# Kernel optimization log

Hardware: AMD Instinct MI355X
Metric: run time of the kernel (lower is better)

Reference implementation:

```python
import jax, jax.numpy as jnp
import numpy as np

H, W = 256, 256
L = 1024
R = 4
B = 64
EPS = 1e-4
FF = (H + W) * R * 4


def setup_inputs() -> dict:
    key = jax.random.key(0)
    ks = jax.random.split(key, 8)
    x = jax.random.normal(ks[0], (B, L), dtype=jnp.float32)
    # Linear weights (torch Linear: out = x @ W.T), kaiming-uniform-ish init
    lim = 1.0 / np.sqrt(L)
    W_t = jax.random.uniform(ks[1], (FF, L), minval=-lim, maxval=lim, dtype=jnp.float32)
    W_g = jax.random.uniform(ks[2], (FF, L), minval=-lim, maxval=lim, dtype=jnp.float32)
    # weights_static: [2, H, W, 2]
    k_lim = np.sqrt(6.0 / (H * W))
    ws0 = jax.random.uniform(ks[3], (1, H, W, 2), minval=-k_lim, maxval=k_lim, dtype=jnp.float32)
    ws1_re = jax.random.uniform(ks[4], (1, H, W, 1), minval=EPS - 1.0, maxval=1.0 - EPS, dtype=jnp.float32)
    ws1_im = jax.random.uniform(ks[5], (1, H, W, 1), minval=-EPS, maxval=EPS, dtype=jnp.float32)
    weights_static = jnp.concatenate([ws0, jnp.concatenate([ws1_re, ws1_im], axis=-1)], axis=0)
    x_lim = np.sqrt(6.0 / (H + W))
    weights_mod = jax.random.uniform(ks[6], (4, H, W), minval=-x_lim, maxval=x_lim, dtype=jnp.float32)
    c_lim = 1.0 / np.sqrt(R)
    kc1, kc2 = jax.random.split(ks[7])
    conv_w = jax.random.uniform(kc1, (R, R), minval=-c_lim, maxval=c_lim, dtype=jnp.float32)  # [out_ch, in_ch] for 1x1 conv
    conv_b = jax.random.uniform(kc2, (R,), minval=-c_lim, maxval=c_lim, dtype=jnp.float32)
    return {"x": x, "W_t": W_t, "W_g": W_g, "weights_static": weights_static,
            "weights_mod": weights_mod, "conv_w": conv_w, "conv_b": conv_b}


def reference(x, W_t, W_g, weights_static, weights_mod, conv_w, conv_b):
    b = x.shape[0]
    xt = x @ W_t.T                                  # [B, FF]
    xg = x @ W_g.T
    xg = xg * jax.nn.sigmoid(xg)                    # SiLU-style gate
    mod = xt * xg
    mod = mod.reshape(b, 4, -1)
    mod = mod / jnp.sqrt(jnp.mean(jnp.abs(mod), axis=-1, keepdims=True) + EPS)
    mod = mod.reshape(b, 4, R, H + W)
    a_part = mod[..., :H]                           # [B,4,R,H]
    b_part = mod[..., H:]                           # [B,4,R,W]
    outer = jnp.einsum('bkri,bkrj->bkrij', a_part, b_part)  # [B,4,R,H,W]
    # 1x1 conv (R->R) followed by sum over output channels collapses to a
    # single contraction with column-summed weights + summed bias (same math).
    w_eff = conv_w.sum(axis=0)                      # [R]
    b_eff = conv_b.sum()
    mod = jnp.einsum('bkrij,r->bkij', outer, w_eff) + b_eff  # [B,4,H,W]
    mod = weights_mod[None] * mod
    A0 = weights_static[0]                          # [H,W,2]
    A1 = weights_static[1]                          # [H,W,2]
    Bc = jnp.moveaxis(mod[:, 0:2], 1, -1)           # [B,H,W,2]
    re = A1[..., 0] * Bc[..., 0] - A1[..., 1] * Bc[..., 1]
    im = A1[..., 0] * Bc[..., 1] - A1[..., 1] * Bc[..., 0]
    mag = jnp.sqrt(re * re + im * im + EPS)         # [B,H,W]
    mag = jnp.sqrt(jnp.mean(mag, axis=(-1, -2)) + EPS)  # [B]
    inv = 1.0 / mag[:, None, None]
    mw_re = A0[..., 0] + re * inv                   # [B,H,W]
    mw_im = A0[..., 1] + im * inv
    proj = jnp.moveaxis(mod[:, 2:4], 1, -1)         # [B,H,W,2]
    den = jnp.sqrt(proj[..., 0] ** 2 + proj[..., 1] ** 2 + EPS)
    theta_cos = proj[..., 0] / den
    theta_sin = proj[..., 1] / den
    return mw_re * theta_cos + mw_im * theta_sin    # [B,H,W]
```

## Files before the change

kernel.cpp:

```cpp
#include <hip/hip_runtime.h>

typedef __bf16 bf16x8 __attribute__((ext_vector_type(8)));
typedef float floatx4 __attribute__((ext_vector_type(4)));

__device__ inline void cvt8_hl(const float* __restrict__ p, bf16x8& h, bf16x8& l){
  float4 v0 = *reinterpret_cast<const float4*>(p);
  float4 v1 = *reinterpret_cast<const float4*>(p + 4);
  float v[8] = {v0.x, v0.y, v0.z, v0.w, v1.x, v1.y, v1.z, v1.w};
  #pragma unroll
  for (int i = 0; i < 8; ++i) {
    __bf16 hi = (__bf16)v[i];
    h[i] = hi;
    l[i] = (__bf16)(v[i] - (float)hi);
  }
}

__global__ __launch_bounds__(256) void k1_gemm(
    const float* __restrict__ x,
    const float* __restrict__ Wt,
    const float* __restrict__ Wg,
    float* __restrict__ mod)
{
  __shared__ float red[3][32][64];
  const int tid  = threadIdx.x;
  const int wave = tid >> 6, lane = tid & 63;
  const int quad = lane >> 4, r16 = lane & 15;
  const int ff = blockIdx.x * 16 + r16;
  const int kb = wave * 256 + quad * 8;

  floatx4 accT[4], accG[4];
  #pragma unroll
  for (int m = 0; m < 4; ++m) { accT[m] = (floatx4)0.0f; accG[m] = (floatx4)0.0f; }

  const float* wt = Wt + ff * 1024 + kb;
  const float* wg = Wg + ff * 1024 + kb;
  const float* xp = x  + r16 * 1024 + kb;

  #pragma unroll
  for (int it = 0; it < 8; ++it) {
    const int ko = it * 32;
    bf16x8 bth, btl, bgh, bgl;
    cvt8_hl(wt + ko, bth, btl);
    cvt8_hl(wg + ko, bgh, bgl);
    #pragma unroll
    for (int mt = 0; mt < 4; ++mt) {
      bf16x8 ah, al;
      cvt8_hl(xp + mt * 16384 + ko, ah, al);
      accT[mt] = __builtin_amdgcn_mfma_f32_16x16x32_bf16(ah, bth, accT[mt], 0, 0, 0);
      accT[mt] = __builtin_amdgcn_mfma_f32_16x16x32_bf16(ah, btl, accT[mt], 0, 0, 0);
      accT[mt] = __builtin_amdgcn_mfma_f32_16x16x32_bf16(al, bth, accT[mt], 0, 0, 0);
      accG[mt] = __builtin_amdgcn_mfma_f32_16x16x32_bf16(ah, bgh, accG[mt], 0, 0, 0);
      accG[mt] = __builtin_amdgcn_mfma_f32_16x16x32_bf16(ah, bgl, accG[mt], 0, 0, 0);
      accG[mt] = __builtin_amdgcn_mfma_f32_16x16x32_bf16(al, bgh, accG[mt], 0, 0, 0);
    }
  }

  if (wave != 0) {
    #pragma unroll
    for (int mt = 0; mt < 4; ++mt)
      #pragma unroll
      for (int r = 0; r < 4; ++r) {
        red[wave - 1][mt * 4 + r][lane]      = accT[mt][r];
        red[wave - 1][16 + mt * 4 + r][lane] = accG[mt][r];
      }
  }
  __syncthreads();
  if (wave == 0) {
    #pragma unroll
    for (int mt = 0; mt < 4; ++mt) {
      #pragma unroll
      for (int r = 0; r < 4; ++r) {
        float t = accT[mt][r] + red[0][mt * 4 + r][lane]
                              + red[1][mt * 4 + r][lane]
                              + red[2][mt * 4 + r][lane];
        float g = accG[mt][r] + red[0][16 + mt * 4 + r][lane]
                              + red[1][16 + mt * 4 + r][lane]
                              + red[2][16 + mt * 4 + r][lane];
        float sig = 1.0f / (1.0f + __expf(-g));
        int b = mt * 16 + quad * 4 + r;
        mod[b * 8192 + ff] = t * g * sig;
      }
    }
  }
}

__global__ __launch_bounds__(256) void k1b_scale(const float* __restrict__ mod,
                                                 float* __restrict__ s)
{
  const int row = blockIdx.x;
  const int tid = threadIdx.x;
  const float* p = mod + row * 2048;
  float sum = 0.0f;
  #pragma unroll
  for (int q = 0; q < 8; ++q) sum += fabsf(p[q * 256 + tid]);
  #pragma unroll
  for (int o = 1; o < 64; o <<= 1) sum += __shfl_xor(sum, o, 64);
  __shared__ float ls[4];
  if ((tid & 63) == 0) ls[tid >> 6] = sum;
  __syncthreads();
  if (tid == 0) {
    float t = ls[0] + ls[1] + ls[2] + ls[3];
    s[row] = rsqrtf(t * (1.0f / 2048.0f) + 1e-4f);
  }
}

__global__ __launch_bounds__(256) void k2_mag(
    const float* __restrict__ mod, const float* __restrict__ s,
    const float* __restrict__ wstat,
    const float* __restrict__ wmod,
    const float* __restrict__ cw,
    const float* __restrict__ cb,
    float* __restrict__ partial)
{
  const int b = blockIdx.x, jc = blockIdx.y;
  const int tid = threadIdx.x;
  __shared__ __align__(16) float a_l[256 * 8];

  float weff[4]; float beff = 0.0f;
  #pragma unroll
  for (int r = 0; r < 4; ++r) {
    weff[r] = cw[r] + cw[4 + r] + cw[8 + r] + cw[12 + r];
    beff += cb[r];
  }
  const float s0 = s[b * 4 + 0], s1 = s[b * 4 + 1];
  const float* mb = mod + b * 8192;

  #pragma unroll
  for (int p = 0; p < 8; ++p) {
    int k = p >> 2, r = p & 3;
    float sc = (k ? s1 : s0) * weff[r];
    a_l[tid * 8 + p] = mb[k * 2048 + r * 512 + tid] * sc;
  }
  const int j = jc * 32 + (tid & 31);
  float bp[8];
  #pragma unroll
  for (int p = 0; p < 8; ++p) {
    int k = p >> 2, r = p & 3;
    bp[p] = mb[k * 2048 + r * 512 + 256 + j] * (k ? s1 : s0);
  }
  __syncthreads();

  const int ioff = tid >> 5;
  float acc = 0.0f;
  for (int it = 0; it < 32; ++it) {
    const int i = it * 8 + ioff;
    const float4 av0 = *reinterpret_cast<const float4*>(&a_l[i * 8]);
    const float4 av1 = *reinterpret_cast<const float4*>(&a_l[i * 8 + 4]);
    float d0 = av0.x * bp[0] + av0.y * bp[1] + av0.z * bp[2] + av0.w * bp[3];
    float d1 = av1.x * bp[4] + av1.y * bp[5] + av1.z * bp[6] + av1.w * bp[7];
    const int ij = i * 256 + j;
    float m0 = wmod[ij] * (d0 + beff);
    float m1 = wmod[65536 + ij] * (d1 + beff);
    float2 a1 = *reinterpret_cast<const float2*>(wstat + 131072 + ij * 2);
    float re = a1.x * m0 - a1.y * m1;
    float im = a1.x * m1 - a1.y * m0;
    acc += sqrtf(re * re + im * im + 1e-4f);
  }
  #pragma unroll
  for (int o = 1; o < 64; o <<= 1) acc += __shfl_xor(acc, o, 64);
  __shared__ float wsum[4];
  if ((tid & 63) == 0) wsum[tid >> 6] = acc;
  __syncthreads();
  if (tid == 0) partial[b * 8 + jc] = wsum[0] + wsum[1] + wsum[2] + wsum[3];
}

__global__ __launch_bounds__(256) void k4_out(
    const float* __restrict__ mod, const float* __restrict__ s,
    const float* __restrict__ wstat,
    const float* __restrict__ wmod,
    const float* __restrict__ cw,
    const float* __restrict__ cb,
    const float* __restrict__ partial,
    float* __restrict__ out)
{
  const int b = blockIdx.x, ibase = blockIdx.y * 32;
  const int tid = threadIdx.x;
  __shared__ __align__(16) float a_l[32 * 16];

  float weff[4]; float beff = 0.0f;
  #pragma unroll
  for (int r = 0; r < 4; ++r) {
    weff[r] = cw[r] + cw[4 + r] + cw[8 + r] + cw[12 + r];
    beff += cb[r];
  }
  float sk[4];
  #pragma unroll
  for (int k = 0; k < 4; ++k) sk[k] = s[b * 4 + k];
  const float* mb = mod + b * 8192;

  float tot = 0.0f;
  #pragma unroll
  for (int t = 0; t < 8; ++t) tot += partial[b * 8 + t];
  const float inv = rsqrtf(tot * (1.0f / 65536.0f) + 1e-4f);

  #pragma unroll
  for (int p = 0; p < 2; ++p) {
    int idx = p * 256 + tid;
    int il = idx & 31, kr = idx >> 5;
    int k = kr >> 2, r = kr & 3;
    a_l[il * 16 + kr] = mb[k * 2048 + r * 512 + ibase + il] * (sk[k] * weff[r]);
  }
  const int j = (tid & 127) * 2;
  const int ioff = tid >> 7;
  float bp0[16], bp1[16];
  #pragma unroll
  for (int kr = 0; kr < 16; ++kr) {
    int k = kr >> 2, r = kr & 3;
    float2 v = *reinterpret_cast<const float2*>(mb + k * 2048 + r * 512 + 256 + j);
    bp0[kr] = v.x * sk[k]; bp1[kr] = v.y * sk[k];
  }
  __syncthreads();

  #pragma unroll 2
  for (int it = 0; it < 16; ++it) {
    const int il = it * 2 + ioff;
    const int i = ibase + il;
    const float4 a0 = *reinterpret_cast<const float4*>(&a_l[il * 16]);
    const float4 a1 = *reinterpret_cast<const float4*>(&a_l[il * 16 + 4]);
    const float4 a2 = *reinterpret_cast<const float4*>(&a_l[il * 16 + 8]);
    const float4 a3 = *reinterpret_cast<const float4*>(&a_l[il * 16 + 12]);
    const int ij = i * 256 + j;
    const float2 wm0 = *reinterpret_cast<const float2*>(wmod + ij);
    const float2 wm1 = *reinterpret_cast<const float2*>(wmod + 65536 + ij);
    const float2 wm2 = *reinterpret_cast<const float2*>(wmod + 131072 + ij);
    const float2 wm3 = *reinterpret_cast<const float2*>(wmod + 196608 + ij);
    const float4 A0v = *reinterpret_cast<const float4*>(wstat + ij * 2);
    const float4 A1v = *reinterpret_cast<const float4*>(wstat + 131072 + ij * 2);
    float outv[2];
    #pragma unroll
    for (int e = 0; e < 2; ++e) {
      const float* bp = e ? bp1 : bp0;
      float d0 = a0.x * bp[0] + a0.y * bp[1] + a0.z * bp[2] + a0.w * bp[3];
      float d1 = a1.x * bp[4] + a1.y * bp[5] + a1.z * bp[6] + a1.w * bp[7];
      float d2 = a2.x * bp[8] + a2.y * bp[9] + a2.z * bp[10] + a2.w * bp[11];
      float d3 = a3.x * bp[12] + a3.y * bp[13] + a3.z * bp[14] + a3.w * bp[15];
      float m0 = (e ? wm0.y : wm0.x) * (d0 + beff);
      float m1 = (e ? wm1.y : wm1.x) * (d1 + beff);
      float m2 = (e ? wm2.y : wm2.x) * (d2 + beff);
      float m3 = (e ? wm3.y : wm3.x) * (d3 + beff);
      float A0r = e ? A0v.z : A0v.x;
      float A0i = e ? A0v.w : A0v.y;
      float A1r = e ? A1v.z : A1v.x;
      float A1i = e ? A1v.w : A1v.y;
      float re = A1r * m0 - A1i * m1;
      float im = A1r * m1 - A1i * m0;
      float mwre = A0r + re * inv;
      float mwim = A0i + im * inv;
      float rd = rsqrtf(m2 * m2 + m3 * m3 + 1e-4f);
      outv[e] = (mwre * m2 + mwim * m3) * rd;
    }
    *reinterpret_cast<float2*>(out + b * 65536 + ij) = make_float2(outv[0], outv[1]);
  }
}

extern "C" void kernel_launch(void* const* d_in, const int* in_sizes, int n_in,
                              void* d_out, int out_size, void* d_ws, size_t ws_size,
                              hipStream_t stream) {
  const float* x     = (const float*)d_in[0];
  const float* Wt    = (const float*)d_in[1];
  const float* Wg    = (const float*)d_in[2];
  const float* wstat = (const float*)d_in[3];
  const float* wmod  = (const float*)d_in[4];
  const float* cw    = (const float*)d_in[5];
  const float* cb    = (const float*)d_in[6];

  float* mod     = (float*)d_ws;
  float* sbuf    = mod + 524288;
  float* partial = sbuf + 256;

  k1_gemm  <<<512, 256, 0, stream>>>(x, Wt, Wg, mod);
  k1b_scale<<<256, 256, 0, stream>>>(mod, sbuf);
  k2_mag   <<<dim3(64, 8), 256, 0, stream>>>(mod, sbuf, wstat, wmod, cw, cb, partial);
  k4_out   <<<dim3(64, 8), 256, 0, stream>>>(mod, sbuf, wstat, wmod, cw, cb, partial,
                                             (float*)d_out);
}
```

Baseline: 152.1 us.

## Stage GEMM weights through LDS with async loads and fuse abs-sum reduction

Restructures the projection GEMM to use 512-thread blocks, where waves split the batch into 4 tiles and K into 2 halves. Weight tiles are loaded into swizzled, double-buffered LDS via global_load_lds, so they are fetched once per block instead of once per wave. The per-row |mod| sums are now accumulated with atomics in the GEMM epilogue, which removes the separate scale kernel. The consumers compute rsqrt themselves, and a memset is added to clear the sums. This cuts one launch and the redundant weight traffic, at the cost of atomics, an extra memset, and order-dependent float summation.

```diff
diff --git a/kernel.cpp b/kernel.cpp
--- a/kernel.cpp
+++ b/kernel.cpp
@@ -3,9 +3,7 @@
 typedef __bf16 bf16x8 __attribute__((ext_vector_type(8)));
 typedef float floatx4 __attribute__((ext_vector_type(4)));
 
-__device__ inline void cvt8_hl(const float* __restrict__ p, bf16x8& h, bf16x8& l){
-  float4 v0 = *reinterpret_cast<const float4*>(p);
-  float4 v1 = *reinterpret_cast<const float4*>(p + 4);
+__device__ inline void cvt8v(float4 v0, float4 v1, bf16x8& h, bf16x8& l){
   float v[8] = {v0.x, v0.y, v0.z, v0.w, v1.x, v1.y, v1.z, v1.w};
   #pragma unroll
   for (int i = 0; i < 8; ++i) {
@@ -15,97 +13,118 @@
   }
 }
 
-__global__ __launch_bounds__(256) void k1_gemm(
+__device__ inline void gload_lds16(const float* g, float* l){
+  __builtin_amdgcn_global_load_lds(
+      (const __attribute__((address_space(1))) unsigned int*)g,
+      (__attribute__((address_space(3))) unsigned int*)l, 16, 0, 0);
+}
+
+__global__ __launch_bounds__(512, 4) void k1_gemm(
     const float* __restrict__ x,
     const float* __restrict__ Wt,
     const float* __restrict__ Wg,
-    float* __restrict__ mod)
+    float* __restrict__ mod,
+    float* __restrict__ sums)
 {
-  __shared__ float red[3][32][64];
-  const int tid  = threadIdx.x;
-  const int wave = tid >> 6, lane = tid & 63;
-  const int quad = lane >> 4, r16 = lane & 15;
-  const int ff = blockIdx.x * 16 + r16;
-  const int kb = wave * 256 + quad * 8;
-
-  floatx4 accT[4], accG[4];
-  #pragma unroll
-  for (int m = 0; m < 4; ++m) { accT[m] = (floatx4)0.0f; accG[m] = (floatx4)0.0f; }
-
-  const float* wt = Wt + ff * 1024 + kb;
-  const float* wg = Wg + ff * 1024 + kb;
-  const float* xp = x  + r16 * 1024 + kb;
-
-  #pragma unroll
-  for (int it = 0; it < 8; ++it) {
-    const int ko = it * 32;
-    bf16x8 bth, btl, bgh, bgl;
-    cvt8_hl(wt + ko, bth, btl);
-    cvt8_hl(wg + ko, bgh, bgl);
-    #pragma unroll
-    for (int mt = 0; mt < 4; ++mt) {
-      bf16x8 ah, al;
-      cvt8_hl(xp + mt * 16384 + ko, ah, al);
-      accT[mt] = __builtin_amdgcn_mfma_f32_16x16x32_bf16(ah, bth, accT[mt], 0, 0, 0);
-      accT[mt] = __builtin_amdgcn_mfma_f32_16x16x32_bf16(ah, btl, accT[mt], 0, 0, 0);
-      accT[mt] = __builtin_amdgcn_mfma_f32_16x16x32_bf16(al, bth, accT[mt], 0, 0, 0);
-      accG[mt] = __builtin_amdgcn_mfma_f32_16x16x32_bf16(ah, bgh, accG[mt], 0, 0, 0);
-      accG[mt] = __builtin_amdgcn_mfma_f32_16x16x32_bf16(ah, bgl, accG[mt], 0, 0, 0);
-      accG[mt] = __builtin_amdgcn_mfma_f32_16x16x32_bf16(al, bgh, accG[mt], 0, 0, 0);
-    }
-  }
-
-  if (wave != 0) {
-    #pragma unroll
-    for (int mt = 0; mt < 4; ++mt)
-      #pragma unroll
-      for (int r = 0; r < 4; ++r) {
-        red[wave - 1][mt * 4 + r][lane]      = accT[mt][r];
-        red[wave - 1][16 + mt * 4 + r][lane] = accG[mt][r];
-      }
-  }
-  __syncthreads();
-  if (wave == 0) {
-    #pragma unroll
-    for (int mt = 0; mt < 4; ++mt) {
-      #pragma unroll
-      for (int r = 0; r < 4; ++r) {
-        float t = accT[mt][r] + red[0][mt * 4 + r][lane]
-                              + red[1][mt * 4 + r][lane]
-                              + red[2][mt * 4 + r][lane];
-        float g = accG[mt][r] + red[0][16 + mt * 4 + r][lane]
-                              + red[1][16 + mt * 4 + r][lane]
-                              + red[2][16 + mt * 4 + r][lane];
-        float sig = 1.0f / (1.0f + __expf(-g));
-        int b = mt * 16 + quad * 4 + r;
-        mod[b * 8192 + ff] = t * g * sig;
-      }
-    }
-  }
-}
-
-__global__ __launch_bounds__(256) void k1b_scale(const float* __restrict__ mod,
-                                                 float* __restrict__ s)
-{
-  const int row = blockIdx.x;
-  const int tid = threadIdx.x;
-  const float* p = mod + row * 2048;
-  float sum = 0.0f;
-  #pragma unroll
-  for (int q = 0; q < 8; ++q) sum += fabsf(p[q * 256 + tid]);
-  #pragma unroll
-  for (int o = 1; o < 64; o <<= 1) sum += __shfl_xor(sum, o, 64);
-  __shared__ float ls[4];
-  if ((tid & 63) == 0) ls[tid >> 6] = sum;
-  __syncthreads();
-  if (tid == 0) {
-    float t = ls[0] + ls[1] + ls[2] + ls[3];
-    s[row] = rsqrtf(t * (1.0f / 2048.0f) + 1e-4f);
+  __shared__ __align__(16) float wlds[2][2][2][16 * 128];
+  __shared__ __align__(16) float red[4][64][8];
+
+  const int tid   = threadIdx.x;
+  const int wave  = tid >> 6, lane = tid & 63;
+  const int wtile = wave & 3;
+  const int khalf = wave >> 2;
+  const int quad  = lane >> 4, r16 = lane & 15;
+  const int ffbase = blockIdx.x * 16;
+  const int kbase  = khalf * 512;
+
+  const int j0 = 2 * wtile, j1 = j0 + 1;
+  const int row0 = 2 * j0 + (lane >> 5);
+  const int row1 = 2 * j1 + (lane >> 5);
+  const int cbyte = (lane & 31) * 16;
+  const int src_f0 = (ffbase + row0) * 1024 + kbase + ((cbyte ^ ((row0 & 7) << 4)) >> 2);
+  const int src_f1 = (ffbase + row1) * 1024 + kbase + ((cbyte ^ ((row1 & 7) << 4)) >> 2);
+
+  const float* xsrc = x + (wtile * 16 + r16) * 1024 + kbase + quad * 8;
+
+  const int rowb = r16 * 512;
+  const int xr   = (r16 & 7) << 4;
+
+  floatx4 accT = (floatx4)0.0f, accG = (floatx4)0.0f;
+
+  auto STAGE = [&](int buf, int kc) {
+    gload_lds16(Wt + src_f0 + kc, &wlds[buf][khalf][0][0] + j0 * 256);
+    gload_lds16(Wt + src_f1 + kc, &wlds[buf][khalf][0][0] + j1 * 256);
+    gload_lds16(Wg + src_f0 + kc, &wlds[buf][khalf][1][0] + j0 * 256);
+    gload_lds16(Wg + src_f1 + kc, &wlds[buf][khalf][1][0] + j1 * 256);
+  };
+
+  STAGE(0, 0);
+  __syncthreads();
+
+  #pragma unroll
+  for (int it = 0; it < 4; ++it) {
+    const int kc = it * 128;
+    float4 xv[4][2];
+    #pragma unroll
+    for (int ks = 0; ks < 4; ++ks) {
+      xv[ks][0] = *reinterpret_cast<const float4*>(xsrc + kc + ks * 32);
+      xv[ks][1] = *reinterpret_cast<const float4*>(xsrc + kc + ks * 32 + 4);
+    }
+    if (it < 3) STAGE((it + 1) & 1, kc + 128);
+
+    const char* tT = (const char*)&wlds[it & 1][khalf][0][0];
+    const char* tG = (const char*)&wlds[it & 1][khalf][1][0];
+    #pragma unroll
+    for (int ks = 0; ks < 4; ++ks) {
+      const int c0  = ks * 128 + quad * 32;
+      const int aLo = rowb + (c0 ^ xr);
+      const int aHi = rowb + ((c0 + 16) ^ xr);
+      bf16x8 ah, al, bth, btl, bgh, bgl;
+      cvt8v(xv[ks][0], xv[ks][1], ah, al);
+      cvt8v(*reinterpret_cast<const float4*>(tT + aLo),
+            *reinterpret_cast<const float4*>(tT + aHi), bth, btl);
+      cvt8v(*reinterpret_cast<const float4*>(tG + aLo),
+            *reinterpret_cast<const float4*>(tG + aHi), bgh, bgl);
+      accT = __builtin_amdgcn_mfma_f32_16x16x32_bf16(ah, bth, accT, 0, 0, 0);
+      accT = __builtin_amdgcn_mfma_f32_16x16x32_bf16(ah, btl, accT, 0, 0, 0);
+      accT = __builtin_amdgcn_mfma_f32_16x16x32_bf16(al, bth, accT, 0, 0, 0);
+      accG = __builtin_amdgcn_mfma_f32_16x16x32_bf16(ah, bgh, accG, 0, 0, 0);
+      accG = __builtin_amdgcn_mfma_f32_16x16x32_bf16(ah, bgl, accG, 0, 0, 0);
+      accG = __builtin_amdgcn_mfma_f32_16x16x32_bf16(al, bgh, accG, 0, 0, 0);
+    }
+    __syncthreads();
+  }
+
+  if (khalf == 1) {
+    #pragma unroll
+    for (int r = 0; r < 4; ++r) {
+      red[wtile][lane][r]     = accT[r];
+      red[wtile][lane][4 + r] = accG[r];
+    }
+  }
+  __syncthreads();
+  if (khalf == 0) {
+    const int kg = ffbase >> 11;
+    #pragma unroll
+    for (int r = 0; r < 4; ++r) {
+      float t = accT[r] + red[wtile][lane][r];
+      float g = accG[r] + red[wtile][lane][4 + r];
+      float sig = 1.0f / (1.0f + __expf(-g));
+      float m = t * g * sig;
+      const int b = wtile * 16 + quad * 4 + r;
+      mod[b * 8192 + ffbase + r16] = m;
+      float a = fabsf(m);
+      a += __shfl_xor(a, 1, 64);
+      a += __shfl_xor(a, 2, 64);
+      a += __shfl_xor(a, 4, 64);
+      a += __shfl_xor(a, 8, 64);
+      if (r16 == 0) atomicAdd(&sums[b * 4 + kg], a);
+    }
   }
 }
 
 __global__ __launch_bounds__(256) void k2_mag(
-    const float* __restrict__ mod, const float* __restrict__ s,
+    const float* __restrict__ mod, const float* __restrict__ sums,
     const float* __restrict__ wstat,
     const float* __restrict__ wmod,
     const float* __restrict__ cw,
@@ -122,7 +141,8 @@
     weff[r] = cw[r] + cw[4 + r] + cw[8 + r] + cw[12 + r];
     beff += cb[r];
   }
-  const float s0 = s[b * 4 + 0], s1 = s[b * 4 + 1];
+  const float s0 = rsqrtf(sums[b * 4 + 0] * (1.0f / 2048.0f) + 1e-4f);
+  const float s1 = rsqrtf(sums[b * 4 + 1] * (1.0f / 2048.0f) + 1e-4f);
   const float* mb = mod + b * 8192;
 
   #pragma unroll
@@ -165,7 +185,7 @@
 }
 
 __global__ __launch_bounds__(256) void k4_out(
-    const float* __restrict__ mod, const float* __restrict__ s,
+    const float* __restrict__ mod, const float* __restrict__ sums,
     const float* __restrict__ wstat,
     const float* __restrict__ wmod,
     const float* __restrict__ cw,
@@ -185,7 +205,8 @@
   }
   float sk[4];
   #pragma unroll
-  for (int k = 0; k < 4; ++k) sk[k] = s[b * 4 + k];
+  for (int k = 0; k < 4; ++k)
+    sk[k] = rsqrtf(sums[b * 4 + k] * (1.0f / 2048.0f) + 1e-4f);
   const float* mb = mod + b * 8192;
 
   float tot = 0.0f;
@@ -265,12 +286,12 @@
   const float* cb    = (const float*)d_in[6];
 
   float* mod     = (float*)d_ws;
-  float* sbuf    = mod + 524288;
-  float* partial = sbuf + 256;
-
-  k1_gemm  <<<512, 256, 0, stream>>>(x, Wt, Wg, mod);
-  k1b_scale<<<256, 256, 0, stream>>>(mod, sbuf);
-  k2_mag   <<<dim3(64, 8), 256, 0, stream>>>(mod, sbuf, wstat, wmod, cw, cb, partial);
-  k4_out   <<<dim3(64, 8), 256, 0, stream>>>(mod, sbuf, wstat, wmod, cw, cb, partial,
-                                             (float*)d_out);
-}
+  float* sums    = mod + 524288;
+  float* partial = sums + 256;
+
+  hipMemsetAsync(sums, 0, 256 * sizeof(float), stream);
+  k1_gemm<<<512, 512, 0, stream>>>(x, Wt, Wg, mod, sums);
+  k2_mag <<<dim3(64, 8), 256, 0, stream>>>(mod, sums, wstat, wmod, cw, cb, partial);
+  k4_out <<<dim3(64, 8), 256, 0, stream>>>(mod, sums, wstat, wmod, cw, cb, partial,
+                                           (float*)d_out);
+}
```

After: 193.3 us. 27.1% more time.

## Fuse abs-mean scale into GEMM epilogue and split downstream kernels finer

Applied to the files above, without the earlier changes.

The GEMM now runs 512-thread blocks with an 8-way K split and a tree reduction in shared memory. Its epilogue computes the per-row abs sums with shuffles and atomics, so the separate scale kernel is removed. The magnitude kernel gains a third grid dimension that splits the i range and accumulates into partial sums with atomics. The output kernel uses 4x more blocks with fewer rows each. This cuts one launch and raises parallelism, at the cost of a memset, atomic contention, and float summation order that is no longer deterministic.

```diff
diff --git a/kernel.cpp b/kernel.cpp
--- a/kernel.cpp
+++ b/kernel.cpp
@@ -15,18 +15,21 @@
   }
 }
 
-__global__ __launch_bounds__(256) void k1_gemm(
+__global__ __launch_bounds__(512, 4) void k1_gemm(
     const float* __restrict__ x,
     const float* __restrict__ Wt,
     const float* __restrict__ Wg,
-    float* __restrict__ mod)
+    float* __restrict__ mod,
+    float* __restrict__ sums)
 {
-  __shared__ float red[3][32][64];
+  __shared__ float red[4 * 64 * 33];
+
   const int tid  = threadIdx.x;
   const int wave = tid >> 6, lane = tid & 63;
   const int quad = lane >> 4, r16 = lane & 15;
-  const int ff = blockIdx.x * 16 + r16;
-  const int kb = wave * 256 + quad * 8;
+  const int ffbase = blockIdx.x * 16;
+  const int ff = ffbase + r16;
+  const int kb = wave * 128 + quad * 8;
 
   floatx4 accT[4], accG[4];
   #pragma unroll
@@ -37,7 +40,7 @@
   const float* xp = x  + r16 * 1024 + kb;
 
   #pragma unroll
-  for (int it = 0; it < 8; ++it) {
+  for (int it = 0; it < 4; ++it) {
     const int ko = it * 32;
     bf16x8 bth, btl, bgh, bgl;
     cvt8_hl(wt + ko, bth, btl);
@@ -55,66 +58,65 @@
     }
   }
 
-  if (wave != 0) {
+  auto tree = [&](int h) {
+    if (wave >= h && wave < 2 * h) {
+      float* dst = &red[((wave - h) * 64 + lane) * 33];
+      #pragma unroll
+      for (int mt = 0; mt < 4; ++mt)
+        #pragma unroll
+        for (int r = 0; r < 4; ++r) {
+          dst[mt * 4 + r]      = accT[mt][r];
+          dst[16 + mt * 4 + r] = accG[mt][r];
+        }
+    }
+    __syncthreads();
+    if (wave < h) {
+      const float* src = &red[(wave * 64 + lane) * 33];
+      #pragma unroll
+      for (int mt = 0; mt < 4; ++mt)
+        #pragma unroll
+        for (int r = 0; r < 4; ++r) {
+          accT[mt][r] += src[mt * 4 + r];
+          accG[mt][r] += src[16 + mt * 4 + r];
+        }
+    }
+    __syncthreads();
+  };
+  tree(4); tree(2); tree(1);
+
+  if (wave == 0) {
+    const int kg = ffbase >> 11;
     #pragma unroll
     for (int mt = 0; mt < 4; ++mt)
       #pragma unroll
       for (int r = 0; r < 4; ++r) {
-        red[wave - 1][mt * 4 + r][lane]      = accT[mt][r];
-        red[wave - 1][16 + mt * 4 + r][lane] = accG[mt][r];
+        float t = accT[mt][r];
+        float g = accG[mt][r];
+        float sig = 1.0f / (1.0f + __expf(-g));
+        float m = t * g * sig;
+        const int b = mt * 16 + quad * 4 + r;
+        mod[b * 8192 + ff] = m;
+        float a = fabsf(m);
+        a += __shfl_xor(a, 1, 64);
+        a += __shfl_xor(a, 2, 64);
+        a += __shfl_xor(a, 4, 64);
+        a += __shfl_xor(a, 8, 64);
+        if (r16 == 0) atomicAdd(&sums[b * 4 + kg], a);
       }
   }
-  __syncthreads();
-  if (wave == 0) {
-    #pragma unroll
-    for (int mt = 0; mt < 4; ++mt) {
-      #pragma unroll
-      for (int r = 0; r < 4; ++r) {
-        float t = accT[mt][r] + red[0][mt * 4 + r][lane]
-                              + red[1][mt * 4 + r][lane]
-                              + red[2][mt * 4 + r][lane];
-        float g = accG[mt][r] + red[0][16 + mt * 4 + r][lane]
-                              + red[1][16 + mt * 4 + r][lane]
-                              + red[2][16 + mt * 4 + r][lane];
-        float sig = 1.0f / (1.0f + __expf(-g));
-        int b = mt * 16 + quad * 4 + r;
-        mod[b * 8192 + ff] = t * g * sig;
-      }
-    }
-  }
-}
-
-__global__ __launch_bounds__(256) void k1b_scale(const float* __restrict__ mod,
-                                                 float* __restrict__ s)
-{
-  const int row = blockIdx.x;
-  const int tid = threadIdx.x;
-  const float* p = mod + row * 2048;
-  float sum = 0.0f;
-  #pragma unroll
-  for (int q = 0; q < 8; ++q) sum += fabsf(p[q * 256 + tid]);
-  #pragma unroll
-  for (int o = 1; o < 64; o <<= 1) sum += __shfl_xor(sum, o, 64);
-  __shared__ float ls[4];
-  if ((tid & 63) == 0) ls[tid >> 6] = sum;
-  __syncthreads();
-  if (tid == 0) {
-    float t = ls[0] + ls[1] + ls[2] + ls[3];
-    s[row] = rsqrtf(t * (1.0f / 2048.0f) + 1e-4f);
-  }
 }
 
 __global__ __launch_bounds__(256) void k2_mag(
-    const float* __restrict__ mod, const float* __restrict__ s,
+    const float* __restrict__ mod, const float* __restrict__ sums,
     const float* __restrict__ wstat,
     const float* __restrict__ wmod,
     const float* __restrict__ cw,
     const float* __restrict__ cb,
     float* __restrict__ partial)
 {
-  const int b = blockIdx.x, jc = blockIdx.y;
+  const int b = blockIdx.x, jc = blockIdx.y, isplit = blockIdx.z;
   const int tid = threadIdx.x;
-  __shared__ __align__(16) float a_l[256 * 8];
+  __shared__ __align__(16) float a_l[64 * 8];
 
   float weff[4]; float beff = 0.0f;
   #pragma unroll
@@ -122,14 +124,16 @@
     weff[r] = cw[r] + cw[4 + r] + cw[8 + r] + cw[12 + r];
     beff += cb[r];
   }
-  const float s0 = s[b * 4 + 0], s1 = s[b * 4 + 1];
+  const float s0 = rsqrtf(sums[b * 4 + 0] * (1.0f / 2048.0f) + 1e-4f);
+  const float s1 = rsqrtf(sums[b * 4 + 1] * (1.0f / 2048.0f) + 1e-4f);
   const float* mb = mod + b * 8192;
 
   #pragma unroll
-  for (int p = 0; p < 8; ++p) {
+  for (int q = 0; q < 2; ++q) {
+    int e = q * 256 + tid;
+    int il = e & 63, p = e >> 6;
     int k = p >> 2, r = p & 3;
-    float sc = (k ? s1 : s0) * weff[r];
-    a_l[tid * 8 + p] = mb[k * 2048 + r * 512 + tid] * sc;
+    a_l[il * 8 + p] = mb[k * 2048 + r * 512 + isplit * 64 + il] * ((k ? s1 : s0) * weff[r]);
   }
   const int j = jc * 32 + (tid & 31);
   float bp[8];
@@ -142,10 +146,12 @@
 
   const int ioff = tid >> 5;
   float acc = 0.0f;
-  for (int it = 0; it < 32; ++it) {
-    const int i = it * 8 + ioff;
-    const float4 av0 = *reinterpret_cast<const float4*>(&a_l[i * 8]);
-    const float4 av1 = *reinterpret_cast<const float4*>(&a_l[i * 8 + 4]);
+  #pragma unroll
+  for (int it = 0; it < 8; ++it) {
+    const int il = it * 8 + ioff;
+    const int i = isplit * 64 + il;
+    const float4 av0 = *reinterpret_cast<const float4*>(&a_l[il * 8]);
+    const float4 av1 = *reinterpret_cast<const float4*>(&a_l[il * 8 + 4]);
     float d0 = av0.x * bp[0] + av0.y * bp[1] + av0.z * bp[2] + av0.w * bp[3];
     float d1 = av1.x * bp[4] + av1.y * bp[5] + av1.z * bp[6] + av1.w * bp[7];
     const int ij = i * 256 + j;
@@ -161,11 +167,11 @@
   __shared__ float wsum[4];
   if ((tid & 63) == 0) wsum[tid >> 6] = acc;
   __syncthreads();
-  if (tid == 0) partial[b * 8 + jc] = wsum[0] + wsum[1] + wsum[2] + wsum[3];
+  if (tid == 0) atomicAdd(&partial[b * 8 + jc], wsum[0] + wsum[1] + wsum[2] + wsum[3]);
 }
 
 __global__ __launch_bounds__(256) void k4_out(
-    const float* __restrict__ mod, const float* __restrict__ s,
+    const float* __restrict__ mod, const float* __restrict__ sums,
     const float* __restrict__ wstat,
     const float* __restrict__ wmod,
     const float* __restrict__ cw,
@@ -173,9 +179,9 @@
     const float* __restrict__ partial,
     float* __restrict__ out)
 {
-  const int b = blockIdx.x, ibase = blockIdx.y * 32;
+  const int b = blockIdx.x, ibase = blockIdx.y * 8;
   const int tid = threadIdx.x;
-  __shared__ __align__(16) float a_l[32 * 16];
+  __shared__ __align__(16) float a_l[8 * 16];
 
   float weff[4]; float beff = 0.0f;
   #pragma unroll
@@ -185,7 +191,8 @@
   }
   float sk[4];
   #pragma unroll
-  for (int k = 0; k < 4; ++k) sk[k] = s[b * 4 + k];
+  for (int k = 0; k < 4; ++k)
+    sk[k] = rsqrtf(sums[b * 4 + k] * (1.0f / 2048.0f) + 1e-4f);
   const float* mb = mod + b * 8192;
 
   float tot = 0.0f;
@@ -193,10 +200,8 @@
   for (int t = 0; t < 8; ++t) tot += partial[b * 8 + t];
   const float inv = rsqrtf(tot * (1.0f / 65536.0f) + 1e-4f);
 
-  #pragma unroll
-  for (int p = 0; p < 2; ++p) {
-    int idx = p * 256 + tid;
-    int il = idx & 31, kr = idx >> 5;
+  if (tid < 128) {
+    int il = tid & 7, kr = tid >> 3;
     int k = kr >> 2, r = kr & 3;
     a_l[il * 16 + kr] = mb[k * 2048 + r * 512 + ibase + il] * (sk[k] * weff[r]);
   }
@@ -211,8 +216,8 @@
   }
   __syncthreads();
 
-  #pragma unroll 2
-  for (int it = 0; it < 16; ++it) {
+  #pragma unroll
+  for (int it = 0; it < 4; ++it) {
     const int il = it * 2 + ioff;
     const int i = ibase + il;
     const float4 a0 = *reinterpret_cast<const float4*>(&a_l[il * 16]);
@@ -265,12 +270,12 @@
   const float* cb    = (const float*)d_in[6];
 
   float* mod     = (float*)d_ws;
-  float* sbuf    = mod + 524288;
-  float* partial = sbuf + 256;
-
-  k1_gemm  <<<512, 256, 0, stream>>>(x, Wt, Wg, mod);
-  k1b_scale<<<256, 256, 0, stream>>>(mod, sbuf);
-  k2_mag   <<<dim3(64, 8), 256, 0, stream>>>(mod, sbuf, wstat, wmod, cw, cb, partial);
-  k4_out   <<<dim3(64, 8), 256, 0, stream>>>(mod, sbuf, wstat, wmod, cw, cb, partial,
-                                             (float*)d_out);
-}
+  float* sums    = mod + 524288;
+  float* partial = sums + 256;
+
+  hipMemsetAsync(sums, 0, (256 + 512) * sizeof(float), stream);
+  k1_gemm<<<512, 512, 0, stream>>>(x, Wt, Wg, mod, sums);
+  k2_mag <<<dim3(64, 8, 4), 256, 0, stream>>>(mod, sums, wstat, wmod, cw, cb, partial);
+  k4_out <<<dim3(64, 32), 256, 0, stream>>>(mod, sums, wstat, wmod, cw, cb, partial,
+                                            (float*)d_out);
+}
```

After: 200.9 us. 1.32x slower.

## Fuse scale, magnitude and output kernels into one cooperative grid-synced kernel

Applied to the files above, without the earlier changes.

Merges the three post-GEMM kernels into a single cooperative kernel of 512 blocks that uses grid-wide syncs between phases. Row sums and magnitude partials are accumulated with atomics into a buffer zeroed by a memset. The magnitude phase now stages the A operand in 64-row LDS chunks instead of all 256 rows. This removes two kernel launches and their inter-kernel gaps, but adds a memset, atomics, and two grid barriers whose cost may approach what the launches cost.

```diff
diff --git a/kernel.cpp b/kernel.cpp
--- a/kernel.cpp
+++ b/kernel.cpp
@@ -1,4 +1,7 @@
 #include <hip/hip_runtime.h>
+#include <hip/hip_cooperative_groups.h>
+
+namespace cg = cooperative_groups;
 
 typedef __bf16 bf16x8 __attribute__((ext_vector_type(8)));
 typedef float floatx4 __attribute__((ext_vector_type(4)));
@@ -84,37 +87,23 @@
   }
 }
 
-__global__ __launch_bounds__(256) void k1b_scale(const float* __restrict__ mod,
-                                                 float* __restrict__ s)
-{
-  const int row = blockIdx.x;
-  const int tid = threadIdx.x;
-  const float* p = mod + row * 2048;
-  float sum = 0.0f;
-  #pragma unroll
-  for (int q = 0; q < 8; ++q) sum += fabsf(p[q * 256 + tid]);
-  #pragma unroll
-  for (int o = 1; o < 64; o <<= 1) sum += __shfl_xor(sum, o, 64);
-  __shared__ float ls[4];
-  if ((tid & 63) == 0) ls[tid >> 6] = sum;
-  __syncthreads();
-  if (tid == 0) {
-    float t = ls[0] + ls[1] + ls[2] + ls[3];
-    s[row] = rsqrtf(t * (1.0f / 2048.0f) + 1e-4f);
-  }
-}
-
-__global__ __launch_bounds__(256) void k2_mag(
-    const float* __restrict__ mod, const float* __restrict__ s,
+__global__ __launch_bounds__(256) void k234(
+    const float* __restrict__ mod,
+    float* __restrict__ sums,
     const float* __restrict__ wstat,
     const float* __restrict__ wmod,
     const float* __restrict__ cw,
     const float* __restrict__ cb,
-    float* __restrict__ partial)
+    float* __restrict__ partial,
+    float* __restrict__ out)
 {
-  const int b = blockIdx.x, jc = blockIdx.y;
+  const int bid = blockIdx.x;
   const int tid = threadIdx.x;
-  __shared__ __align__(16) float a_l[256 * 8];
+  const int wave = tid >> 6;
+
+  __shared__ float ls[4];
+  __shared__ __align__(16) float a2l[64 * 8];
+  __shared__ __align__(16) float a4l[32 * 16];
 
   float weff[4]; float beff = 0.0f;
   #pragma unroll
@@ -122,134 +111,141 @@
     weff[r] = cw[r] + cw[4 + r] + cw[8 + r] + cw[12 + r];
     beff += cb[r];
   }
-  const float s0 = s[b * 4 + 0], s1 = s[b * 4 + 1];
-  const float* mb = mod + b * 8192;
-
-  #pragma unroll
-  for (int p = 0; p < 8; ++p) {
-    int k = p >> 2, r = p & 3;
-    float sc = (k ? s1 : s0) * weff[r];
-    a_l[tid * 8 + p] = mb[k * 2048 + r * 512 + tid] * sc;
-  }
-  const int j = jc * 32 + (tid & 31);
-  float bp[8];
-  #pragma unroll
-  for (int p = 0; p < 8; ++p) {
-    int k = p >> 2, r = p & 3;
-    bp[p] = mb[k * 2048 + r * 512 + 256 + j] * (k ? s1 : s0);
-  }
-  __syncthreads();
-
-  const int ioff = tid >> 5;
-  float acc = 0.0f;
-  for (int it = 0; it < 32; ++it) {
-    const int i = it * 8 + ioff;
-    const float4 av0 = *reinterpret_cast<const float4*>(&a_l[i * 8]);
-    const float4 av1 = *reinterpret_cast<const float4*>(&a_l[i * 8 + 4]);
-    float d0 = av0.x * bp[0] + av0.y * bp[1] + av0.z * bp[2] + av0.w * bp[3];
-    float d1 = av1.x * bp[4] + av1.y * bp[5] + av1.z * bp[6] + av1.w * bp[7];
-    const int ij = i * 256 + j;
-    float m0 = wmod[ij] * (d0 + beff);
-    float m1 = wmod[65536 + ij] * (d1 + beff);
-    float2 a1 = *reinterpret_cast<const float2*>(wstat + 131072 + ij * 2);
-    float re = a1.x * m0 - a1.y * m1;
-    float im = a1.x * m1 - a1.y * m0;
-    acc += sqrtf(re * re + im * im + 1e-4f);
-  }
-  #pragma unroll
-  for (int o = 1; o < 64; o <<= 1) acc += __shfl_xor(acc, o, 64);
-  __shared__ float wsum[4];
-  if ((tid & 63) == 0) wsum[tid >> 6] = acc;
-  __syncthreads();
-  if (tid == 0) partial[b * 8 + jc] = wsum[0] + wsum[1] + wsum[2] + wsum[3];
-}
-
-__global__ __launch_bounds__(256) void k4_out(
-    const float* __restrict__ mod, const float* __restrict__ s,
-    const float* __restrict__ wstat,
-    const float* __restrict__ wmod,
-    const float* __restrict__ cw,
-    const float* __restrict__ cb,
-    const float* __restrict__ partial,
-    float* __restrict__ out)
-{
-  const int b = blockIdx.x, ibase = blockIdx.y * 32;
-  const int tid = threadIdx.x;
-  __shared__ __align__(16) float a_l[32 * 16];
-
-  float weff[4]; float beff = 0.0f;
-  #pragma unroll
-  for (int r = 0; r < 4; ++r) {
-    weff[r] = cw[r] + cw[4 + r] + cw[8 + r] + cw[12 + r];
-    beff += cb[r];
-  }
-  float sk[4];
-  #pragma unroll
-  for (int k = 0; k < 4; ++k) sk[k] = s[b * 4 + k];
-  const float* mb = mod + b * 8192;
-
-  float tot = 0.0f;
-  #pragma unroll
-  for (int t = 0; t < 8; ++t) tot += partial[b * 8 + t];
-  const float inv = rsqrtf(tot * (1.0f / 65536.0f) + 1e-4f);
-
-  #pragma unroll
-  for (int p = 0; p < 2; ++p) {
-    int idx = p * 256 + tid;
-    int il = idx & 31, kr = idx >> 5;
-    int k = kr >> 2, r = kr & 3;
-    a_l[il * 16 + kr] = mb[k * 2048 + r * 512 + ibase + il] * (sk[k] * weff[r]);
-  }
-  const int j = (tid & 127) * 2;
-  const int ioff = tid >> 7;
-  float bp0[16], bp1[16];
-  #pragma unroll
-  for (int kr = 0; kr < 16; ++kr) {
-    int k = kr >> 2, r = kr & 3;
-    float2 v = *reinterpret_cast<const float2*>(mb + k * 2048 + r * 512 + 256 + j);
-    bp0[kr] = v.x * sk[k]; bp1[kr] = v.y * sk[k];
-  }
-  __syncthreads();
-
-  #pragma unroll 2
-  for (int it = 0; it < 16; ++it) {
-    const int il = it * 2 + ioff;
-    const int i = ibase + il;
-    const float4 a0 = *reinterpret_cast<const float4*>(&a_l[il * 16]);
-    const float4 a1 = *reinterpret_cast<const float4*>(&a_l[il * 16 + 4]);
-    const float4 a2 = *reinterpret_cast<const float4*>(&a_l[il * 16 + 8]);
-    const float4 a3 = *reinterpret_cast<const float4*>(&a_l[il * 16 + 12]);
-    const int ij = i * 256 + j;
-    const float2 wm0 = *reinterpret_cast<const float2*>(wmod + ij);
-    const float2 wm1 = *reinterpret_cast<const float2*>(wmod + 65536 + ij);
-    const float2 wm2 = *reinterpret_cast<const float2*>(wmod + 131072 + ij);
-    const float2 wm3 = *reinterpret_cast<const float2*>(wmod + 196608 + ij);
-    const float4 A0v = *reinterpret_cast<const float4*>(wstat + ij * 2);
-    const float4 A1v = *reinterpret_cast<const float4*>(wstat + 131072 + ij * 2);
-    float outv[2];
-    #pragma unroll
-    for (int e = 0; e < 2; ++e) {
-      const float* bp = e ? bp1 : bp0;
-      float d0 = a0.x * bp[0] + a0.y * bp[1] + a0.z * bp[2] + a0.w * bp[3];
-      float d1 = a1.x * bp[4] + a1.y * bp[5] + a1.z * bp[6] + a1.w * bp[7];
-      float d2 = a2.x * bp[8] + a2.y * bp[9] + a2.z * bp[10] + a2.w * bp[11];
-      float d3 = a3.x * bp[12] + a3.y * bp[13] + a3.z * bp[14] + a3.w * bp[15];
-      float m0 = (e ? wm0.y : wm0.x) * (d0 + beff);
-      float m1 = (e ? wm1.y : wm1.x) * (d1 + beff);
-      float m2 = (e ? wm2.y : wm2.x) * (d2 + beff);
-      float m3 = (e ? wm3.y : wm3.x) * (d3 + beff);
-      float A0r = e ? A0v.z : A0v.x;
-      float A0i = e ? A0v.w : A0v.y;
-      float A1r = e ? A1v.z : A1v.x;
-      float A1i = e ? A1v.w : A1v.y;
-      float re = A1r * m0 - A1i * m1;
-      float im = A1r * m1 - A1i * m0;
-      float mwre = A0r + re * inv;
-      float mwim = A0i + im * inv;
-      float rd = rsqrtf(m2 * m2 + m3 * m3 + 1e-4f);
-      outv[e] = (mwre * m2 + mwim * m3) * rd;
-    }
-    *reinterpret_cast<float2*>(out + b * 65536 + ij) = make_float2(outv[0], outv[1]);
+
+  {
+    const int row = bid >> 1, half = bid & 1;
+    const float4 v = *reinterpret_cast<const float4*>(
+        mod + row * 2048 + half * 1024 + tid * 4);
+    float sum = fabsf(v.x) + fabsf(v.y) + fabsf(v.z) + fabsf(v.w);
+    #pragma unroll
+    for (int o = 1; o < 64; o <<= 1) sum += __shfl_xor(sum, o, 64);
+    if ((tid & 63) == 0) ls[wave] = sum;
+    __syncthreads();
+    if (tid == 0) atomicAdd(&sums[row], ls[0] + ls[1] + ls[2] + ls[3]);
+  }
+  cg::this_grid().sync();
+
+  {
+    const int b = bid & 63, jc = bid >> 6;
+    const float s0 = rsqrtf(sums[b * 4 + 0] * (1.0f / 2048.0f) + 1e-4f);
+    const float s1 = rsqrtf(sums[b * 4 + 1] * (1.0f / 2048.0f) + 1e-4f);
+    const float* mb = mod + b * 8192;
+    const int j = jc * 32 + (tid & 31);
+    float bp[8];
+    #pragma unroll
+    for (int p = 0; p < 8; ++p) {
+      int k = p >> 2, r = p & 3;
+      bp[p] = mb[k * 2048 + r * 512 + 256 + j] * (k ? s1 : s0);
+    }
+    float accv = 0.0f;
+    for (int isp = 0; isp < 4; ++isp) {
+      __syncthreads();
+      #pragma unroll
+      for (int q = 0; q < 2; ++q) {
+        int e = q * 256 + tid;
+        int il = e & 63, p = e >> 6;
+        int k = p >> 2, r = p & 3;
+        a2l[il * 8 + p] = mb[k * 2048 + r * 512 + isp * 64 + il]
+                          * ((k ? s1 : s0) * weff[r]);
+      }
+      __syncthreads();
+      const int ioff = tid >> 5;
+      #pragma unroll
+      for (int it = 0; it < 8; ++it) {
+        const int il = it * 8 + ioff;
+        const int i = isp * 64 + il;
+        const float4 av0 = *reinterpret_cast<const float4*>(&a2l[il * 8]);
+        const float4 av1 = *reinterpret_cast<const float4*>(&a2l[il * 8 + 4]);
+        float d0 = av0.x * bp[0] + av0.y * bp[1] + av0.z * bp[2] + av0.w * bp[3];
+        float d1 = av1.x * bp[4] + av1.y * bp[5] + av1.z * bp[6] + av1.w * bp[7];
+        const int ij = i * 256 + j;
+        float m0 = wmod[ij] * (d0 + beff);
+        float m1 = wmod[65536 + ij] * (d1 + beff);
+        float2 a1 = *reinterpret_cast<const float2*>(wstat + 131072 + ij * 2);
+        float re = a1.x * m0 - a1.y * m1;
+        float im = a1.x * m1 - a1.y * m0;
+        accv += sqrtf(re * re + im * im + 1e-4f);
+      }
+    }
+    #pragma unroll
+    for (int o = 1; o < 64; o <<= 1) accv += __shfl_xor(accv, o, 64);
+    __syncthreads();
+    if ((tid & 63) == 0) ls[wave] = accv;
+    __syncthreads();
+    if (tid == 0) atomicAdd(&partial[b * 8 + jc], ls[0] + ls[1] + ls[2] + ls[3]);
+  }
+  cg::this_grid().sync();
+
+  {
+    const int b = bid & 63, ibase = (bid >> 6) * 32;
+    const float* mb = mod + b * 8192;
+    float sk[4];
+    #pragma unroll
+    for (int k = 0; k < 4; ++k)
+      sk[k] = rsqrtf(sums[b * 4 + k] * (1.0f / 2048.0f) + 1e-4f);
+    float tot = 0.0f;
+    #pragma unroll
+    for (int t = 0; t < 8; ++t) tot += partial[b * 8 + t];
+    const float inv = rsqrtf(tot * (1.0f / 65536.0f) + 1e-4f);
+
+    #pragma unroll
+    for (int p = 0; p < 2; ++p) {
+      int idx = p * 256 + tid;
+      int il = idx & 31, kr = idx >> 5;
+      int k = kr >> 2, r = kr & 3;
+      a4l[il * 16 + kr] = mb[k * 2048 + r * 512 + ibase + il] * (sk[k] * weff[r]);
+    }
+    const int j = (tid & 127) * 2;
+    const int ioff = tid >> 7;
+    float bp0[16], bp1[16];
+    #pragma unroll
+    for (int kr = 0; kr < 16; ++kr) {
+      int k = kr >> 2, r = kr & 3;
+      float2 v = *reinterpret_cast<const float2*>(mb + k * 2048 + r * 512 + 256 + j);
+      bp0[kr] = v.x * sk[k]; bp1[kr] = v.y * sk[k];
+    }
+    __syncthreads();
+
+    #pragma unroll 2
+    for (int it = 0; it < 16; ++it) {
+      const int il = it * 2 + ioff;
+      const int i = ibase + il;
+      const float4 a0 = *reinterpret_cast<const float4*>(&a4l[il * 16]);
+      const float4 a1 = *reinterpret_cast<const float4*>(&a4l[il * 16 + 4]);
+      const float4 a2 = *reinterpret_cast<const float4*>(&a4l[il * 16 + 8]);
+      const float4 a3 = *reinterpret_cast<const float4*>(&a4l[il * 16 + 12]);
+      const int ij = i * 256 + j;
+      const float2 wm0 = *reinterpret_cast<const float2*>(wmod + ij);
+      const float2 wm1 = *reinterpret_cast<const float2*>(wmod + 65536 + ij);
+      const float2 wm2 = *reinterpret_cast<const float2*>(wmod + 131072 + ij);
+      const float2 wm3 = *reinterpret_cast<const float2*>(wmod + 196608 + ij);
+      const float4 A0v = *reinterpret_cast<const float4*>(wstat + ij * 2);
+      const float4 A1v = *reinterpret_cast<const float4*>(wstat + 131072 + ij * 2);
+      float outv[2];
+      #pragma unroll
+      for (int e = 0; e < 2; ++e) {
+        const float* bp = e ? bp1 : bp0;
+        float d0 = a0.x * bp[0] + a0.y * bp[1] + a0.z * bp[2] + a0.w * bp[3];
+        float d1 = a1.x * bp[4] + a1.y * bp[5] + a1.z * bp[6] + a1.w * bp[7];
+        float d2 = a2.x * bp[8] + a2.y * bp[9] + a2.z * bp[10] + a2.w * bp[11];
+        float d3 = a3.x * bp[12] + a3.y * bp[13] + a3.z * bp[14] + a3.w * bp[15];
+        float m0 = (e ? wm0.y : wm0.x) * (d0 + beff);
+        float m1 = (e ? wm1.y : wm1.x) * (d1 + beff);
+        float m2 = (e ? wm2.y : wm2.x) * (d2 + beff);
+        float m3 = (e ? wm3.y : wm3.x) * (d3 + beff);
+        float A0r = e ? A0v.z : A0v.x;
+        float A0i = e ? A0v.w : A0v.y;
+        float A1r = e ? A1v.z : A1v.x;
+        float A1i = e ? A1v.w : A1v.y;
+        float re = A1r * m0 - A1i * m1;
+        float im = A1r * m1 - A1i * m0;
+        float mwre = A0r + re * inv;
+        float mwim = A0i + im * inv;
+        float rd = rsqrtf(m2 * m2 + m3 * m3 + 1e-4f);
+        outv[e] = (mwre * m2 + mwim * m3) * rd;
+      }
+      *reinterpret_cast<float2*>(out + b * 65536 + ij) = make_float2(outv[0], outv[1]);
+    }
   }
 }
 
@@ -265,12 +261,14 @@
   const float* cb    = (const float*)d_in[6];
 
   float* mod     = (float*)d_ws;
-  float* sbuf    = mod + 524288;
-  float* partial = sbuf + 256;
-
-  k1_gemm  <<<512, 256, 0, stream>>>(x, Wt, Wg, mod);
-  k1b_scale<<<256, 256, 0, stream>>>(mod, sbuf);
-  k2_mag   <<<dim3(64, 8), 256, 0, stream>>>(mod, sbuf, wstat, wmod, cw, cb, partial);
-  k4_out   <<<dim3(64, 8), 256, 0, stream>>>(mod, sbuf, wstat, wmod, cw, cb, partial,
-                                             (float*)d_out);
-}
+  float* sums    = mod + 524288;
+  float* partial = sums + 256;
+  float* outp    = (float*)d_out;
+
+  hipMemsetAsync(sums, 0, (256 + 512) * sizeof(float), stream);
+  k1_gemm<<<512, 256, 0, stream>>>(x, Wt, Wg, mod);
+
+  void* args[] = {&mod, &sums, &wstat, &wmod, &cw, &cb, &partial, &outp};
+  hipLaunchCooperativeKernel((const void*)k234, dim3(512), dim3(256),
+                             args, 0, stream);
+}
```

After: 252.4 us. 1.66x slower.
